# Optimization experiments

Hardware: AMD Instinct MI355X
Metric: run time of the kernel (lower is better)

The kernel has to match this reference:

```python
import jax, jax.numpy as jnp
import numpy as np

# module hyperparameters (from init_kwargs)
RR = 8          # number of rotating time-trace slots
PFRAC = 0.3     # potentiation fraction
GMAX = 1.0
GMIN = 0.1
TAU = 100.0     # decay time constant
SPKRANGE = 512  # number of spikes per sample
SN = 128        # batch of samples
P, H, W = 2, 128, 128  # polarity, sensor height, sensor width (hard-coded in source)


def setup_inputs() -> dict:
    key = jax.random.key(0)
    kx, ky, kp, kt, ktt, kl = jax.random.split(key, 6)
    x = jax.random.randint(kx, (SN, SPKRANGE), 0, H)
    y = jax.random.randint(ky, (SN, SPKRANGE), 0, W)
    pol = jax.random.randint(kp, (SN, SPKRANGE), 0, P)
    event = jnp.stack([x, y, pol], axis=-1).astype(jnp.int32)  # [SN, SPK, 3] -> (x, y, polarity)
    # monotonically increasing spike timestamps (float path of event[:, :, 3])
    ts = jnp.sort(jax.random.uniform(kt, (SN, SPKRANGE), dtype=jnp.float32) * 5000.0, axis=1)
    tt = jax.random.randint(ktt, (SN, SPKRANGE), 0, RR).astype(jnp.int32)
    tt = tt.at[:, 0].set(0)  # first spike is written to slot 0, matching the torch init
    length = jax.random.randint(kl, (SN,), 1, SPKRANGE).astype(jnp.int32)
    return {"event": event, "ts": ts, "time_trace": tt, "length": length}


def _forward(event, ts, time_trace, length):
    sidx = jnp.arange(SN)
    T2G = jnp.zeros((SN, RR, P, H, W), dtype=ts.dtype)
    # initial spike deposit into slot 0
    x0, y0, p0 = event[:, 0, 0], event[:, 0, 1], event[:, 0, 2]
    T2G = T2G.at[sidx, 0, p0, x0, y0].add(PFRAC * (GMAX - GMIN))

    def step(T2G, xs):
        ev, dt, tprev, tcur, n = xs  # ev:[SN,3], dt:[SN], tprev/tcur:[SN], n: step index
        m = jnp.exp(dt / TAU)  # exp((t[N-1]-t[N])/TAU), dt <= 0
        # gather previous slot slice: [SN, P, H, W]
        prev = jnp.take_along_axis(T2G, tprev[:, None, None, None, None], axis=1)[:, 0]
        new = m[:, None, None, None] * (prev - GMIN) + GMIN  # decay toward GMIN
        # conditional scatter-add potentiation at the spiking pixel
        old = new[sidx, ev[:, 2], ev[:, 0], ev[:, 1]]
        add = jnp.where(length > n, PFRAC * (GMAX - old), 0.0)
        new = new.at[sidx, ev[:, 2], ev[:, 0], ev[:, 1]].add(add)
        # scatter the updated slice into the current slot
        T2G = T2G.at[sidx, tcur].set(new)
        return T2G, None

    xs = (jnp.moveaxis(event[:, 1:], 1, 0),      # [SPK-1, SN, 3]
          (ts[:, :-1] - ts[:, 1:]).T,            # [SPK-1, SN] time deltas (t[N-1]-t[N])
          time_trace[:, :-1].T,                  # previous slot per step
          time_trace[:, 1:].T,                   # current slot per step
          jnp.arange(1, SPKRANGE))               # step index N
    T2G, _ = jax.lax.scan(step, T2G, xs)
    # MaxPool3d((1,2,2), stride (1,2,2)) over (P, H, W)
    pooled = T2G.reshape(SN, RR, P, H // 2, 2, W // 2, 2).max(axis=(4, 6))
    return pooled  # [SN, RR, 2, 64, 64]


def reference(event, ts, time_trace, length):
    return _forward(event, ts, time_trace, length)
```

## Files before the change

### kernel.cpp

```cpp
#include <hip/hip_runtime.h>

#define SN 128
#define SPK 512

constexpr float GMIN  = 0.1f;
constexpr float PFRAC = 0.3f;
constexpr float GMAX  = 1.0f;


__global__ __launch_bounds__(512, 4) void fuse_kernel(
    const int*   __restrict__ event,
    const float* __restrict__ ts,
    const int*   __restrict__ tt,
    const int*   __restrict__ length,
    float*       __restrict__ out)
{
    __shared__ int      tile[2 * 64 * 64];
    __shared__ unsigned lpk [SPK];
    __shared__ float    lCr [SPK];
    __shared__ int      snl [8];
    __shared__ int      wcnt[8];
    __shared__ float    sCs;

    unsigned* hcnt = (unsigned*)tile;

    const int blk  = blockIdx.x;
    const int s    = blk >> 3;
    const int r    = blk & 7;
    const int t    = threadIdx.x;
    const int lane = t & 63;
    const int wid  = t >> 6;

    const int   len = length[s];
    const float ts0 = ts[s * SPK];

    const int* ev = event + (size_t)(s * SPK + t) * 3;
    const int   ex  = ev[0], ey = ev[1], ep = ev[2];
    const float tsn = ts[s * SPK + t];
    const int   tv  = tt[s * SPK + t];

    if (t < 8) snl[t] = -1;
#pragma unroll
    for (int k = 0; k < 8; ++k) hcnt[t + k * 512] = 0u;
    __syncthreads();

    const bool     gate = (t < len);
    const unsigned key  = (unsigned)((ep << 14) | (ex << 7) | ey);
    const float    d    = (ts0 - tsn) * 0.01f;
    const float    myCr = (PFRAC * (GMAX - GMIN)) * __expf(-d);
    const unsigned h    = (key * 2654435761u) >> 20;
    if (t >= 1) atomicMax(&snl[tv], t);
    if (gate)   atomicAdd(&hcnt[h], 1u);
    __syncthreads();

    int nr = snl[r];
    if (r == 0 && nr < 0) nr = 0;
    const bool amb = gate && (hcnt[h] > 1u);
    if (t == nr) sCs = __expf((ts0 - tsn) * 0.01f);
    const unsigned long long bmask = __ballot(amb);
    if (lane == 0) wcnt[wid] = (int)__popcll(bmask);
    __syncthreads();

    int base = 0, nA = 0;
#pragma unroll
    for (int w = 0; w < 8; ++w) {
        int c = wcnt[w];
        if (w < wid) base += c;
        nA += c;
    }
    if (amb) {
        int pos = base + (int)__popcll(bmask & ((1ull << lane) - 1ull));
        lpk[pos] = ((unsigned)t << 16) | key;
        lCr[pos] = myCr;
    }
    const float C_r = (nr >= 0) ? sCs : 0.0f;
    const int   ub  = __float_as_int((nr >= 0) ? (GMIN - C_r * GMIN) : 0.0f);
#pragma unroll
    for (int k = 0; k < 16; ++k) tile[t + k * 512] = ub;
    __syncthreads();

    if (gate && t <= nr) {
        float a = -GMIN;
        if (amb) {
            for (int i = 0; i < nA; ++i) {
                unsigned e = lpk[i];
                if ((e & 0xFFFFu) == key && (e >> 16) < (unsigned)t)
                    a = ((e >> 16) == 0u)
                            ? (PFRAC * (GMAX - GMIN) - GMIN)
                            : fmaf(1.0f - PFRAC, a, lCr[i]);
            }
        }
        a = (t == 0) ? (PFRAC * (GMAX - GMIN) - GMIN)
                     : fmaf(1.0f - PFRAC, a, myCr);
        float val = fmaf(C_r, a, GMIN);
        int   idx = (ep * 64 + (ex >> 1)) * 64 + (ey >> 1);
        atomicMax(&tile[idx], __float_as_int(val));
    }
    __syncthreads();

    float4*       o4 = reinterpret_cast<float4*>(out + (size_t)(s * 8 + r) * 8192);
    const float4* t4 = reinterpret_cast<const float4*>(tile);
#pragma unroll
    for (int k = 0; k < 4; ++k) o4[t + k * 512] = t4[t + k * 512];
}

extern "C" void kernel_launch(void* const* d_in, const int* in_sizes, int n_in,
                              void* d_out, int out_size, void* d_ws, size_t ws_size,
                              hipStream_t stream) {
    const int*   event  = (const int*)  d_in[0];
    const float* ts     = (const float*)d_in[1];
    const int*   tt     = (const int*)  d_in[2];
    const int*   length = (const int*)  d_in[3];
    float*       out    = (float*)d_out;

    fuse_kernel<<<dim3(SN * 8), dim3(512), 0, stream>>>(event, ts, tt, length, out);
}
```

Measured before the change: 16.85 us.

## Split each slot block by polarity with 256 threads handling two spikes each

The grid doubles so each block produces one polarity plane (4096 floats) of one sample/slot, using 256 threads that each process two spikes. The shared tile halves and the output store uses nontemporal vector stores. The C coefficient is now computed by thread 0 from a shared timestamp array instead of by the matching thread. The aim is a smaller LDS footprint and more blocks for higher occupancy and parallelism. In exchange, the per-block setup (event loads, hashing, collision compaction) is duplicated across twice as many blocks.

```diff
diff --git a/kernel.cpp b/kernel.cpp
--- a/kernel.cpp
+++ b/kernel.cpp
@@ -7,26 +7,31 @@
 constexpr float PFRAC = 0.3f;
 constexpr float GMAX  = 1.0f;
 
+typedef float  nfloat4 __attribute__((ext_vector_type(4)));
 
-__global__ __launch_bounds__(512, 4) void fuse_kernel(
+
+__global__ __launch_bounds__(256, 4) void fuse_kernel(
     const int*   __restrict__ event,
     const float* __restrict__ ts,
     const int*   __restrict__ tt,
     const int*   __restrict__ length,
     float*       __restrict__ out)
 {
-    __shared__ int      tile[2 * 64 * 64];
+    __shared__ int      tile[4096];
+    __shared__ float    stsn[SPK];
     __shared__ unsigned lpk [SPK];
     __shared__ float    lCr [SPK];
     __shared__ int      snl [8];
     __shared__ int      wcnt[8];
-    __shared__ float    sCs;
+    __shared__ float    sCx;
+    __shared__ int      sNrx;
 
     unsigned* hcnt = (unsigned*)tile;
 
     const int blk  = blockIdx.x;
-    const int s    = blk >> 3;
-    const int r    = blk & 7;
+    const int s    = blk >> 4;
+    const int r    = (blk >> 1) & 7;
+    const int p    = blk & 1;
     const int t    = threadIdx.x;
     const int lane = t & 63;
     const int wid  = t >> 6;
@@ -34,74 +39,110 @@
     const int   len = length[s];
     const float ts0 = ts[s * SPK];
 
-    const int* ev = event + (size_t)(s * SPK + t) * 3;
-    const int   ex  = ev[0], ey = ev[1], ep = ev[2];
-    const float tsn = ts[s * SPK + t];
-    const int   tv  = tt[s * SPK + t];
+#pragma unroll
+    for (int k = 0; k < 16; ++k) hcnt[t + k * 256] = 0u;
+    if (t < 8) snl[t] = -1;
 
-    if (t < 8) snl[t] = -1;
+    int ex[2], ey[2], ep[2], tv[2]; float tsn[2], myCr[2];
+    bool gate[2]; unsigned key[2], h[2];
 #pragma unroll
-    for (int k = 0; k < 8; ++k) hcnt[t + k * 512] = 0u;
+    for (int q = 0; q < 2; ++q) {
+        int n = t + q * 256;
+        const int* ev = event + (size_t)(s * SPK + n) * 3;
+        ex[q] = ev[0]; ey[q] = ev[1]; ep[q] = ev[2];
+        tsn[q]  = ts[s * SPK + n];
+        tv[q]   = tt[s * SPK + n];
+        gate[q] = (n < len);
+        key[q]  = (unsigned)((ep[q] << 14) | (ex[q] << 7) | ey[q]);
+        h[q]    = (key[q] * 2654435761u) >> 20;
+        myCr[q] = (PFRAC * (GMAX - GMIN)) * __expf(-(ts0 - tsn[q]) * 0.01f);
+    }
     __syncthreads();
 
-    const bool     gate = (t < len);
-    const unsigned key  = (unsigned)((ep << 14) | (ex << 7) | ey);
-    const float    d    = (ts0 - tsn) * 0.01f;
-    const float    myCr = (PFRAC * (GMAX - GMIN)) * __expf(-d);
-    const unsigned h    = (key * 2654435761u) >> 20;
-    if (t >= 1) atomicMax(&snl[tv], t);
-    if (gate)   atomicAdd(&hcnt[h], 1u);
+#pragma unroll
+    for (int q = 0; q < 2; ++q) {
+        int n = t + q * 256;
+        stsn[n] = tsn[q];
+        if (n >= 1)  atomicMax(&snl[tv[q]], n);
+        if (gate[q]) atomicAdd(&hcnt[h[q]], 1u);
+    }
     __syncthreads();
 
-    int nr = snl[r];
-    if (r == 0 && nr < 0) nr = 0;
-    const bool amb = gate && (hcnt[h] > 1u);
-    if (t == nr) sCs = __expf((ts0 - tsn) * 0.01f);
-    const unsigned long long bmask = __ballot(amb);
-    if (lane == 0) wcnt[wid] = (int)__popcll(bmask);
+    bool amb[2];
+    unsigned long long bm[2];
+#pragma unroll
+    for (int q = 0; q < 2; ++q) {
+        amb[q] = gate[q] && (hcnt[h[q]] > 1u);
+        bm[q]  = __ballot(amb[q]);
+        if (lane == 0) wcnt[q * 4 + wid] = (int)__popcll(bm[q]);
+    }
+    if (t == 0) {
+        int nr = snl[r];
+        if (r == 0 && nr < 0) nr = 0;
+        float C = 0.0f;
+        if (nr >= 0) C = __expf((ts0 - stsn[nr]) * 0.01f);
+        sNrx = nr; sCx = C;
+    }
     __syncthreads();
 
-    int base = 0, nA = 0;
+    int base0 = 0, base1 = 0, nA = 0;
 #pragma unroll
     for (int w = 0; w < 8; ++w) {
         int c = wcnt[w];
-        if (w < wid) base += c;
+        if (w < wid)     base0 += c;
+        if (w < 4 + wid) base1 += c;
         nA += c;
     }
-    if (amb) {
-        int pos = base + (int)__popcll(bmask & ((1ull << lane) - 1ull));
-        lpk[pos] = ((unsigned)t << 16) | key;
-        lCr[pos] = myCr;
+    const unsigned long long lmask = (1ull << lane) - 1ull;
+    if (amb[0]) {
+        int pos = base0 + (int)__popcll(bm[0] & lmask);
+        lpk[pos] = ((unsigned)t << 16) | key[0];
+        lCr[pos] = myCr[0];
     }
-    const float C_r = (nr >= 0) ? sCs : 0.0f;
+    if (amb[1]) {
+        int pos = base1 + (int)__popcll(bm[1] & lmask);
+        lpk[pos] = ((unsigned)(t + 256) << 16) | key[1];
+        lCr[pos] = myCr[1];
+    }
+    const int   nr  = sNrx;
+    const float C_r = sCx;
     const int   ub  = __float_as_int((nr >= 0) ? (GMIN - C_r * GMIN) : 0.0f);
+    {
+        int4 u4; u4.x = u4.y = u4.z = u4.w = ub;
+        int4* T = (int4*)tile;
 #pragma unroll
-    for (int k = 0; k < 16; ++k) tile[t + k * 512] = ub;
-    __syncthreads();
-
-    if (gate && t <= nr) {
-        float a = -GMIN;
-        if (amb) {
-            for (int i = 0; i < nA; ++i) {
-                unsigned e = lpk[i];
-                if ((e & 0xFFFFu) == key && (e >> 16) < (unsigned)t)
-                    a = ((e >> 16) == 0u)
-                            ? (PFRAC * (GMAX - GMIN) - GMIN)
-                            : fmaf(1.0f - PFRAC, a, lCr[i]);
-            }
-        }
-        a = (t == 0) ? (PFRAC * (GMAX - GMIN) - GMIN)
-                     : fmaf(1.0f - PFRAC, a, myCr);
-        float val = fmaf(C_r, a, GMIN);
-        int   idx = (ep * 64 + (ex >> 1)) * 64 + (ey >> 1);
-        atomicMax(&tile[idx], __float_as_int(val));
+        for (int k = 0; k < 4; ++k) T[t + k * 256] = u4;
     }
     __syncthreads();
 
-    float4*       o4 = reinterpret_cast<float4*>(out + (size_t)(s * 8 + r) * 8192);
-    const float4* t4 = reinterpret_cast<const float4*>(tile);
 #pragma unroll
-    for (int k = 0; k < 4; ++k) o4[t + k * 512] = t4[t + k * 512];
+    for (int q = 0; q < 2; ++q) {
+        int n = t + q * 256;
+        if (gate[q] && ep[q] == p && n <= nr) {
+            float a = -GMIN;
+            if (amb[q]) {
+                for (int i = 0; i < nA; ++i) {
+                    unsigned e = lpk[i];
+                    if ((e & 0xFFFFu) == key[q] && (e >> 16) < (unsigned)n)
+                        a = ((e >> 16) == 0u)
+                                ? (PFRAC * (GMAX - GMIN) - GMIN)
+                                : fmaf(1.0f - PFRAC, a, lCr[i]);
+                }
+            }
+            a = (n == 0) ? (PFRAC * (GMAX - GMIN) - GMIN)
+                         : fmaf(1.0f - PFRAC, a, myCr[q]);
+            float val = fmaf(C_r, a, GMIN);
+            int   idx = ((ex[q] >> 1) * 64) + (ey[q] >> 1);
+            atomicMax(&tile[idx], __float_as_int(val));
+        }
+    }
+    __syncthreads();
+
+    nfloat4*       o4 = (nfloat4*)(out + (size_t)(((s * 8 + r) * 2 + p)) * 4096);
+    const nfloat4* t4 = (const nfloat4*)tile;
+#pragma unroll
+    for (int k = 0; k < 4; ++k)
+        __builtin_nontemporal_store(t4[t + k * 256], o4 + t + k * 256);
 }
 
 extern "C" void kernel_launch(void* const* d_in, const int* in_sizes, int n_in,
@@ -113,5 +154,5 @@
     const int*   length = (const int*)  d_in[3];
     float*       out    = (float*)d_out;
 
-    fuse_kernel<<<dim3(SN * 8), dim3(512), 0, stream>>>(event, ts, tt, length, out);
+    fuse_kernel<<<dim3(SN * 8 * 2), dim3(256), 0, stream>>>(event, ts, tt, length, out);
 }
```

Result: slower. 20.28 us (+20.3%).
